# Performance work log

Hardware: AMD Instinct MI355X
Metric: run time of the kernel (lower is better)

## Reference

```python
import jax, jax.numpy as jnp
import numpy as np

SCALING = 16.0  # lora_alpha
R = 16


def setup_inputs() -> dict:
    key = jax.random.key(0)
    ks = jax.random.split(key, 6)
    B, S, D_IN, D_OUT = 4, 2048, 4096, 4096
    x = jax.random.normal(ks[0], (B, S, D_IN), dtype=jnp.float32)
    W = jax.random.normal(ks[1], (D_OUT, D_IN), dtype=jnp.float32) * 0.02
    b = jax.random.normal(ks[2], (D_OUT,), dtype=jnp.float32) * 0.02
    lora_A = jax.random.normal(ks[3], (R, D_IN), dtype=jnp.float32) * 0.02
    lora_B = jax.random.normal(ks[4], (D_OUT, R), dtype=jnp.float32) * 0.02
    lora_c = jax.random.uniform(ks[5], (R, 1), dtype=jnp.float32)
    return {"x": x, "W": W, "b": b, "lora_A": lora_A, "lora_B": lora_B, "lora_c": lora_c}


def reference(x, W, b, lora_A, lora_B, lora_c):
    # Base (quantized-in-torch, dense here) linear: x @ W.T + b
    result = jnp.einsum("bsi,oi->bso", x, W) + b
    # LoRA correction: x @ (A * c).T @ B.T * scaling / r
    # Contract down to rank-r first to avoid a [D_IN, D_OUT] intermediate.
    A_scaled = lora_A * lora_c                       # [r, D_IN]
    h = jnp.einsum("bsi,ri->bsr", x, A_scaled)       # [B, S, r] (small)
    lora_out = jnp.einsum("bsr,or->bso", h, lora_B) * (SCALING / R)
    return result + lora_out
```

## Files before the change

### kernel.cpp

```cpp
#include <hip/hip_runtime.h>
#include <hip/hip_bf16.h>
#include <stdint.h>
#include <stddef.h>

#define D_IN   4096
#define D_OUT  4096
#define M_TOT  8192
#define R_RANK 16
#define LORA_SCALE 1.0f

typedef __attribute__((ext_vector_type(8))) short short8;
typedef __attribute__((ext_vector_type(4))) short short4v;
typedef __attribute__((ext_vector_type(4))) float f32x4;

#define GL2LDS16(g, l)                                                  \
  __builtin_amdgcn_global_load_lds(                                     \
      (const __attribute__((address_space(1))) void*)(g),               \
      (__attribute__((address_space(3))) void*)(l), 16, 0, 0)

__global__ __launch_bounds__(256) void prep_w(
    const float* __restrict__ W, const float* __restrict__ A,
    const float* __restrict__ c, const float* __restrict__ B,
    __hip_bfloat16* __restrict__ Wp) {
  int t  = threadIdx.x;
  int i  = blockIdx.x * 1024 + t * 4;
  int o0 = blockIdx.y * 4;

  float4 a4[R_RANK];
#pragma unroll
  for (int r = 0; r < R_RANK; r++) {
    float4 v = *(const float4*)(A + r * D_IN + i);
    float cr = c[r] * LORA_SCALE;
    v.x *= cr; v.y *= cr; v.z *= cr; v.w *= cr;
    a4[r] = v;
  }
#pragma unroll
  for (int oo = 0; oo < 4; oo++) {
    int o = o0 + oo;
    float4 w = *(const float4*)(W + (size_t)o * D_IN + i);
#pragma unroll
    for (int r = 0; r < R_RANK; r++) {
      float br = B[o * R_RANK + r];
      w.x += br * a4[r].x; w.y += br * a4[r].y;
      w.z += br * a4[r].z; w.w += br * a4[r].w;
    }
    __hip_bfloat16 tb[4];
    tb[0] = __float2bfloat16(w.x); tb[1] = __float2bfloat16(w.y);
    tb[2] = __float2bfloat16(w.z); tb[3] = __float2bfloat16(w.w);
    *(short4v*)(Wp + (size_t)o * D_IN + i) = *(const short4v*)tb;
  }
}

__global__ __launch_bounds__(256) void pack_x(
    const float* __restrict__ x, __hip_bfloat16* __restrict__ Xp) {
  size_t idx = ((size_t)blockIdx.x * 256 + threadIdx.x) * 8;
  float4 v0 = *(const float4*)(x + idx);
  float4 v1 = *(const float4*)(x + idx + 4);
  __hip_bfloat16 t[8];
  t[0] = __float2bfloat16(v0.x); t[1] = __float2bfloat16(v0.y);
  t[2] = __float2bfloat16(v0.z); t[3] = __float2bfloat16(v0.w);
  t[4] = __float2bfloat16(v1.x); t[5] = __float2bfloat16(v1.y);
  t[6] = __float2bfloat16(v1.z); t[7] = __float2bfloat16(v1.w);
  *(short8*)(Xp + idx) = *(const short8*)t;
}

#define BK 64
#define NT (D_IN / BK)

#define SOFF(BUFI, AB, KH) ((((BUFI) * 2 + (AB)) * 2 + (KH)) * 8192)

#define VMCNT(N) asm volatile("s_waitcnt vmcnt(" #N ")" ::: "memory")
#define HARD_BARRIER() asm volatile("s_barrier" ::: "memory")
#define SOFT_BARRIER() __builtin_amdgcn_s_barrier()

#define STAGE_HALF(BUFI, AB, KH, TS)                                         \
  do {                                                                       \
    const __hip_bfloat16* _src = (AB) ? Wp : Xp;                             \
    const int _rb = (AB) ? n0 : m0;                                          \
    const int _kb = (TS) * BK + (KH) * 32;                                   \
    _Pragma("unroll")                                                        \
    for (int _is = 0; _is < 2; ++_is) {                                      \
      const int _p = _is * 512 + tid;                     \
      const int _row = _p >> 2;                                              \
      const int _c = (_p & 3) ^ ((_row >> 1) & 3);      \
      GL2LDS16(_src + (size_t)(_rb + _row) * D_IN + _kb + _c * 8,            \
               smem + SOFF(BUFI, AB, KH) + _p * 8);                          \
    }                                                                        \
  } while (0)

#define LOAD_AF(BUFI, KH, MH)                                                \
  _Pragma("unroll")                                                          \
  for (int _j = 0; _j < 4; ++_j)                                             \
    af[_j] = *(const short8*)(smem + SOFF(BUFI, 0, KH) +                     \
                              (wm * 128 + ((MH) * 4 + _j) * 16 + l15) * 32 + \
                              cph * 8);

#define LOAD_BF(BUFI, KH)                                                    \
  _Pragma("unroll")                                                          \
  for (int _nn = 0; _nn < 4; ++_nn)                                          \
    bf[_nn] = *(const short8*)(smem + SOFF(BUFI, 1, KH) +                    \
                               (wn * 64 + _nn * 16 + l15) * 32 + cph * 8);

#define MFMA_HALF(MH)                                                        \
  do {                                                                       \
    __builtin_amdgcn_s_setprio(1);                                           \
    _Pragma("unroll")                                                        \
    for (int _j = 0; _j < 4; ++_j)                                           \
      _Pragma("unroll")                                                      \
      for (int _nn = 0; _nn < 4; ++_nn)                                      \
        acc[(MH) * 4 + _j][_nn] = __builtin_amdgcn_mfma_f32_16x16x32_bf16(   \
            af[_j], bf[_nn], acc[(MH) * 4 + _j][_nn], 0, 0, 0);              \
    __builtin_amdgcn_s_setprio(0);                                           \
  } while (0)

#define TILE_BODY(BUFI, NBUF, T, DO_STAGE)                                   \
  do {                                                                       \
                                                        \
    LOAD_AF(BUFI, 0, 0);                                                     \
    LOAD_BF(BUFI, 0);                                                        \
    if (DO_STAGE) STAGE_HALF(NBUF, 0, 0, (T) + 1);                           \
    SOFT_BARRIER();                                                          \
    MFMA_HALF(0);                                                            \
    SOFT_BARRIER();                                                          \
                                                        \
    LOAD_AF(BUFI, 0, 1);                                                     \
    if (DO_STAGE) STAGE_HALF(NBUF, 1, 0, (T) + 1);                           \
    SOFT_BARRIER();                                                          \
    MFMA_HALF(1);                                                            \
    if (DO_STAGE) { VMCNT(4); } else { VMCNT(0); }                           \
    HARD_BARRIER();                                                          \
                                                        \
    LOAD_AF(BUFI, 1, 0);                                                     \
    LOAD_BF(BUFI, 1);                                                        \
    if (DO_STAGE) STAGE_HALF(NBUF, 0, 1, (T) + 1);                           \
    SOFT_BARRIER();                                                          \
    MFMA_HALF(0);                                                            \
    SOFT_BARRIER();                                                          \
                                                        \
    LOAD_AF(BUFI, 1, 1);                                                     \
    if (DO_STAGE) STAGE_HALF(NBUF, 1, 1, (T) + 1);                           \
    SOFT_BARRIER();                                                          \
    MFMA_HALF(1);                                                            \
    if (DO_STAGE) { VMCNT(4); } else { VMCNT(0); }                           \
    HARD_BARRIER();                                                          \
  } while (0)

__global__ __launch_bounds__(512, 2) void gemm_256(
    const __hip_bfloat16* __restrict__ Xp,
    const __hip_bfloat16* __restrict__ Wp,
    const float* __restrict__ bias,
    float* __restrict__ out) {
  __shared__ __align__(16) __hip_bfloat16 smem[2 * 2 * 2 * 8192];

  const int tid  = threadIdx.x;
  const int wid  = tid >> 6;
  const int lane = tid & 63;
  const int wm = wid >> 2;
  const int wn = wid & 3;
  const int l15 = lane & 15;
  const int kg  = lane >> 4;
  const int cph = kg ^ ((l15 >> 1) & 3);
  const int m0 = blockIdx.y * 256;
  const int n0 = blockIdx.x * 256;

  f32x4 acc[8][4];
#pragma unroll
  for (int i = 0; i < 8; i++)
#pragma unroll
    for (int j = 0; j < 4; j++) acc[i][j] = (f32x4){0.f, 0.f, 0.f, 0.f};

  short8 af[4];
  short8 bf[4];

  STAGE_HALF(0, 0, 0, 0);
  STAGE_HALF(0, 1, 0, 0);
  STAGE_HALF(0, 0, 1, 0);
  STAGE_HALF(0, 1, 1, 0);
  VMCNT(4);
  HARD_BARRIER();

#pragma unroll 1
  for (int t = 0; t < NT - 2; t += 2) {
    TILE_BODY(0, 1, t, 1);
    TILE_BODY(1, 0, t + 1, 1);
  }
  TILE_BODY(0, 1, NT - 2, 1);
  TILE_BODY(1, 0, NT - 1, 0);

  float bv[4];
#pragma unroll
  for (int nn = 0; nn < 4; ++nn) bv[nn] = bias[n0 + wn * 64 + nn * 16 + l15];
#pragma unroll
  for (int mm = 0; mm < 8; ++mm) {
#pragma unroll
    for (int reg = 0; reg < 4; ++reg) {
      const int row = m0 + wm * 128 + mm * 16 + kg * 4 + reg;
      float* po = out + (size_t)row * D_OUT + n0 + wn * 64 + l15;
#pragma unroll
      for (int nn = 0; nn < 4; ++nn) po[nn * 16] = acc[mm][nn][reg] + bv[nn];
    }
  }
}

extern "C" void kernel_launch(void* const* d_in, const int* in_sizes, int n_in,
                              void* d_out, int out_size, void* d_ws, size_t ws_size,
                              hipStream_t stream) {
  const float* x  = (const float*)d_in[0];
  const float* W  = (const float*)d_in[1];
  const float* b  = (const float*)d_in[2];
  const float* lA = (const float*)d_in[3];
  const float* lB = (const float*)d_in[4];
  const float* lc = (const float*)d_in[5];
  float* out = (float*)d_out;

  char* ws = (char*)d_ws;
  __hip_bfloat16* Xp = (__hip_bfloat16*)ws;
  __hip_bfloat16* Wp = (__hip_bfloat16*)(ws + (size_t)67108864);

  pack_x<<<dim3(M_TOT * D_IN / (256 * 8)), dim3(256), 0, stream>>>(x, Xp);
  prep_w<<<dim3(D_IN / 1024, D_OUT / 4), dim3(256), 0, stream>>>(W, lA, lc, lB, Wp);
  gemm_256<<<dim3(D_OUT / 256, M_TOT / 256), dim3(512), 0, stream>>>(Xp, Wp, b, out);
}
```

Baseline: 501.3 us.

## Switch GEMM to 32x32x16 MFMA with fragment-ordered LDS layout; fuse prep kernels

Replaces the 16x16x32 bf16 MFMA tiling with 32x32x16 MFMAs. The LDS staging layout is reorganised so that each wave reads its A and B fragments as contiguous 512-element chunks indexed by lane, and the epilogue is rewritten to match the 32x32 accumulator mapping. The intent is fewer MFMA issues, fewer LDS reads per FLOP, and conflict-free fragment loads without XOR swizzling. Separately, the x-pack and W-prep kernels are merged into one launch with a block-index split to cut one kernel launch and overlap their tails. The larger accumulators and the new layout change register pressure and global-load coalescing patterns.

After: 558.5 us. 1.11x slower.

```diff
diff --git a/kernel.cpp b/kernel.cpp
--- a/kernel.cpp
+++ b/kernel.cpp
@@ -11,20 +11,37 @@
 
 typedef __attribute__((ext_vector_type(8))) short short8;
 typedef __attribute__((ext_vector_type(4))) short short4v;
-typedef __attribute__((ext_vector_type(4))) float f32x4;
+typedef __attribute__((ext_vector_type(16))) float f32x16;
 
 #define GL2LDS16(g, l)                                                  \
   __builtin_amdgcn_global_load_lds(                                     \
       (const __attribute__((address_space(1))) void*)(g),               \
       (__attribute__((address_space(3))) void*)(l), 16, 0, 0)
 
-__global__ __launch_bounds__(256) void prep_w(
+#define PACK_BLOCKS 16384
+#define PREP_BLOCKS 4096
+
+__global__ __launch_bounds__(256) void pack_prep(
+    const float* __restrict__ x, __hip_bfloat16* __restrict__ Xp,
     const float* __restrict__ W, const float* __restrict__ A,
     const float* __restrict__ c, const float* __restrict__ B,
     __hip_bfloat16* __restrict__ Wp) {
+  if (blockIdx.x < PACK_BLOCKS) {
+    size_t idx = ((size_t)blockIdx.x * 256 + threadIdx.x) * 8;
+    float4 v0 = *(const float4*)(x + idx);
+    float4 v1 = *(const float4*)(x + idx + 4);
+    __hip_bfloat16 t[8];
+    t[0] = __float2bfloat16(v0.x); t[1] = __float2bfloat16(v0.y);
+    t[2] = __float2bfloat16(v0.z); t[3] = __float2bfloat16(v0.w);
+    t[4] = __float2bfloat16(v1.x); t[5] = __float2bfloat16(v1.y);
+    t[6] = __float2bfloat16(v1.z); t[7] = __float2bfloat16(v1.w);
+    *(short8*)(Xp + idx) = *(const short8*)t;
+    return;
+  }
+  int bid = blockIdx.x - PACK_BLOCKS;
   int t  = threadIdx.x;
-  int i  = blockIdx.x * 1024 + t * 4;
-  int o0 = blockIdx.y * 4;
+  int i  = (bid & 3) * 1024 + t * 4;
+  int o0 = (bid >> 2) * 4;
 
   float4 a4[R_RANK];
 #pragma unroll
@@ -51,19 +68,6 @@
   }
 }
 
-__global__ __launch_bounds__(256) void pack_x(
-    const float* __restrict__ x, __hip_bfloat16* __restrict__ Xp) {
-  size_t idx = ((size_t)blockIdx.x * 256 + threadIdx.x) * 8;
-  float4 v0 = *(const float4*)(x + idx);
-  float4 v1 = *(const float4*)(x + idx + 4);
-  __hip_bfloat16 t[8];
-  t[0] = __float2bfloat16(v0.x); t[1] = __float2bfloat16(v0.y);
-  t[2] = __float2bfloat16(v0.z); t[3] = __float2bfloat16(v0.w);
-  t[4] = __float2bfloat16(v1.x); t[5] = __float2bfloat16(v1.y);
-  t[6] = __float2bfloat16(v1.z); t[7] = __float2bfloat16(v1.w);
-  *(short8*)(Xp + idx) = *(const short8*)t;
-}
-
 #define BK 64
 #define NT (D_IN / BK)
 
@@ -73,74 +77,79 @@
 #define HARD_BARRIER() asm volatile("s_barrier" ::: "memory")
 #define SOFT_BARRIER() __builtin_amdgcn_s_barrier()
 
-#define STAGE_HALF(BUFI, AB, KH, TS)                                         \
+#define STAGE_HALF(BUFI, AB, H, TS)                                          \
   do {                                                                       \
     const __hip_bfloat16* _src = (AB) ? Wp : Xp;                             \
-    const int _rb = (AB) ? n0 : m0;                                          \
-    const int _kb = (TS) * BK + (KH) * 32;                                   \
+    const int _rb0 = (AB) ? n0 : m0;                                         \
     _Pragma("unroll")                                                        \
     for (int _is = 0; _is < 2; ++_is) {                                      \
-      const int _p = _is * 512 + tid;                     \
-      const int _row = _p >> 2;                                              \
-      const int _c = (_p & 3) ^ ((_row >> 1) & 3);      \
-      GL2LDS16(_src + (size_t)(_rb + _row) * D_IN + _kb + _c * 8,            \
-               smem + SOFF(BUFI, AB, KH) + _p * 8);                          \
+      const int _p = _is * 512 + tid;                           \
+      const int _s = _p >> 6;                                 \
+      const int _j = _p & 63;                          \
+      const int _row = (_s & 7) * 32 + (_j & 31);                            \
+      const int _k = ((H) * 2 + (_s >> 3)) * 16 + (_j >> 5) * 8;             \
+      GL2LDS16(_src + (size_t)(_rb0 + _row) * D_IN + (TS) * BK + _k,         \
+               smem + SOFF(BUFI, AB, H) + _p * 8);                           \
     }                                                                        \
   } while (0)
 
-#define LOAD_AF(BUFI, KH, MH)                                                \
+#define LOAD_AF(BUFI, H, RH)                                                 \
   _Pragma("unroll")                                                          \
-  for (int _j = 0; _j < 4; ++_j)                                             \
-    af[_j] = *(const short8*)(smem + SOFF(BUFI, 0, KH) +                     \
-                              (wm * 128 + ((MH) * 4 + _j) * 16 + l15) * 32 + \
-                              cph * 8);
-
-#define LOAD_BF(BUFI, KH)                                                    \
+  for (int _i = 0; _i < 4; ++_i)                                             \
+    af[_i] = *(const short8*)(smem + SOFF(BUFI, 0, H) +                      \
+                              ((_i >> 1) * 8 + wm * 4 + (RH) * 2 +           \
+                               (_i & 1)) * 512 + lane * 8);
+
+#define LOAD_BF(BUFI, H)                                                     \
   _Pragma("unroll")                                                          \
-  for (int _nn = 0; _nn < 4; ++_nn)                                          \
-    bf[_nn] = *(const short8*)(smem + SOFF(BUFI, 1, KH) +                    \
-                               (wn * 64 + _nn * 16 + l15) * 32 + cph * 8);
-
-#define MFMA_HALF(MH)                                                        \
+  for (int _i = 0; _i < 4; ++_i)                                             \
+    bf[_i] = *(const short8*)(smem + SOFF(BUFI, 1, H) +                      \
+                              ((_i >> 1) * 8 + wn * 2 + (_i & 1)) * 512 +    \
+                              lane * 8);
+
+#define MFMA_QUAD(RH)                                                        \
   do {                                                                       \
     __builtin_amdgcn_s_setprio(1);                                           \
     _Pragma("unroll")                                                        \
-    for (int _j = 0; _j < 4; ++_j)                                           \
+    for (int _kfh = 0; _kfh < 2; ++_kfh)                                     \
       _Pragma("unroll")                                                      \
-      for (int _nn = 0; _nn < 4; ++_nn)                                      \
-        acc[(MH) * 4 + _j][_nn] = __builtin_amdgcn_mfma_f32_16x16x32_bf16(   \
-            af[_j], bf[_nn], acc[(MH) * 4 + _j][_nn], 0, 0, 0);              \
+      for (int _r = 0; _r < 2; ++_r)                                         \
+        _Pragma("unroll")                                                    \
+        for (int _n = 0; _n < 2; ++_n)                                       \
+          acc[(RH) * 2 + _r][_n] = __builtin_amdgcn_mfma_f32_32x32x16_bf16(  \
+              af[_kfh * 2 + _r], bf[_kfh * 2 + _n],                          \
+              acc[(RH) * 2 + _r][_n], 0, 0, 0);                              \
     __builtin_amdgcn_s_setprio(0);                                           \
   } while (0)
 
 #define TILE_BODY(BUFI, NBUF, T, DO_STAGE)                                   \
   do {                                                                       \
-                                                        \
+                                                  \
     LOAD_AF(BUFI, 0, 0);                                                     \
     LOAD_BF(BUFI, 0);                                                        \
     if (DO_STAGE) STAGE_HALF(NBUF, 0, 0, (T) + 1);                           \
     SOFT_BARRIER();                                                          \
-    MFMA_HALF(0);                                                            \
-    SOFT_BARRIER();                                                          \
-                                                        \
+    MFMA_QUAD(0);                                                            \
+    SOFT_BARRIER();                                                          \
+                                                  \
     LOAD_AF(BUFI, 0, 1);                                                     \
     if (DO_STAGE) STAGE_HALF(NBUF, 1, 0, (T) + 1);                           \
     SOFT_BARRIER();                                                          \
-    MFMA_HALF(1);                                                            \
+    MFMA_QUAD(1);                                                            \
     if (DO_STAGE) { VMCNT(4); } else { VMCNT(0); }                           \
     HARD_BARRIER();                                                          \
-                                                        \
+                                                  \
     LOAD_AF(BUFI, 1, 0);                                                     \
     LOAD_BF(BUFI, 1);                                                        \
     if (DO_STAGE) STAGE_HALF(NBUF, 0, 1, (T) + 1);                           \
     SOFT_BARRIER();                                                          \
-    MFMA_HALF(0);                                                            \
-    SOFT_BARRIER();                                                          \
-                                                        \
+    MFMA_QUAD(0);                                                            \
+    SOFT_BARRIER();                                                          \
+                                                  \
     LOAD_AF(BUFI, 1, 1);                                                     \
     if (DO_STAGE) STAGE_HALF(NBUF, 1, 1, (T) + 1);                           \
     SOFT_BARRIER();                                                          \
-    MFMA_HALF(1);                                                            \
+    MFMA_QUAD(1);                                                            \
     if (DO_STAGE) { VMCNT(4); } else { VMCNT(0); }                           \
     HARD_BARRIER();                                                          \
   } while (0)
@@ -157,17 +166,18 @@
   const int lane = tid & 63;
   const int wm = wid >> 2;
   const int wn = wid & 3;
-  const int l15 = lane & 15;
-  const int kg  = lane >> 4;
-  const int cph = kg ^ ((l15 >> 1) & 3);
+  const int l31 = lane & 31;
+  const int lh  = lane >> 5;
   const int m0 = blockIdx.y * 256;
   const int n0 = blockIdx.x * 256;
 
-  f32x4 acc[8][4];
-#pragma unroll
-  for (int i = 0; i < 8; i++)
-#pragma unroll
-    for (int j = 0; j < 4; j++) acc[i][j] = (f32x4){0.f, 0.f, 0.f, 0.f};
+  f32x16 acc[4][2];
+#pragma unroll
+  for (int i = 0; i < 4; i++)
+#pragma unroll
+    for (int j = 0; j < 2; j++)
+#pragma unroll
+      for (int k = 0; k < 16; k++) acc[i][j][k] = 0.f;
 
   short8 af[4];
   short8 bf[4];
@@ -187,17 +197,17 @@
   TILE_BODY(0, 1, NT - 2, 1);
   TILE_BODY(1, 0, NT - 1, 0);
 
-  float bv[4];
-#pragma unroll
-  for (int nn = 0; nn < 4; ++nn) bv[nn] = bias[n0 + wn * 64 + nn * 16 + l15];
-#pragma unroll
-  for (int mm = 0; mm < 8; ++mm) {
-#pragma unroll
-    for (int reg = 0; reg < 4; ++reg) {
-      const int row = m0 + wm * 128 + mm * 16 + kg * 4 + reg;
-      float* po = out + (size_t)row * D_OUT + n0 + wn * 64 + l15;
-#pragma unroll
-      for (int nn = 0; nn < 4; ++nn) po[nn * 16] = acc[mm][nn][reg] + bv[nn];
+  float bv[2];
+#pragma unroll
+  for (int nb = 0; nb < 2; ++nb) bv[nb] = bias[n0 + wn * 64 + nb * 32 + l31];
+#pragma unroll
+  for (int rb = 0; rb < 4; ++rb) {
+#pragma unroll
+    for (int r = 0; r < 16; ++r) {
+      const int row = m0 + wm * 128 + rb * 32 + (r & 3) + 8 * (r >> 2) + 4 * lh;
+      float* po = out + (size_t)row * D_OUT + n0 + wn * 64 + l31;
+      po[0]  = acc[rb][0][r] + bv[0];
+      po[32] = acc[rb][1][r] + bv[1];
     }
   }
 }
@@ -217,7 +227,7 @@
   __hip_bfloat16* Xp = (__hip_bfloat16*)ws;
   __hip_bfloat16* Wp = (__hip_bfloat16*)(ws + (size_t)67108864);
 
-  pack_x<<<dim3(M_TOT * D_IN / (256 * 8)), dim3(256), 0, stream>>>(x, Xp);
-  prep_w<<<dim3(D_IN / 1024, D_OUT / 4), dim3(256), 0, stream>>>(W, lA, lc, lB, Wp);
+  pack_prep<<<dim3(PACK_BLOCKS + PREP_BLOCKS), dim3(256), 0, stream>>>(
+      x, Xp, W, lA, lc, lB, Wp);
   gemm_256<<<dim3(D_OUT / 256, M_TOT / 256), dim3(512), 0, stream>>>(Xp, Wp, b, out);
 }
```
